# Performance work log

Hardware: AMD Instinct MI355X
Metric: run time of the kernel (lower is better)

## Reference

```python
import jax, jax.numpy as jnp
import numpy as np
from jax import lax

INPUT = 99
HIDDEN = 64
T = 65536


def setup_inputs() -> dict:
    key = jax.random.key(0)
    ks = jax.random.split(key, 8)
    x = jax.random.normal(ks[0], (1, T, INPUT), dtype=jnp.float32)
    # PyTorch LSTM params: weight_ih_l0 [4H, in], weight_hh_l0 [4H, H], biases [4H]
    s = 1.0 / np.sqrt(HIDDEN)
    W_ih = jax.random.uniform(ks[1], (4 * HIDDEN, INPUT), jnp.float32, -s, s)
    W_hh = jax.random.uniform(ks[2], (4 * HIDDEN, HIDDEN), jnp.float32, -s, s)
    b_ih = jax.random.uniform(ks[3], (4 * HIDDEN,), jnp.float32, -s, s)
    b_hh = jax.random.uniform(ks[4], (4 * HIDDEN,), jnp.float32, -s, s)
    # head: Linear(64->32, bias=False), Linear(32->3, bias=True)
    W1 = jax.random.normal(ks[5], (32, HIDDEN), dtype=jnp.float32) * 0.01
    W2 = jax.random.normal(ks[6], (3, 32), dtype=jnp.float32) * 0.01
    b2 = jnp.zeros((3,), dtype=jnp.float32)
    return {"x": x, "W_ih": W_ih, "W_hh": W_hh, "b_ih": b_ih, "b_hh": b_hh,
            "W1": W1, "W2": W2, "b2": b2}


def reference(x, W_ih, W_hh, b_ih, b_hh, W1, W2, b2):
    H = HIDDEN
    # Precompute input projections for all timesteps (one big GEMM).
    # x: [1, T, 99] -> xz: [T, 4H]; x[-1] == last (only) batch row.
    xz = jnp.einsum('td,gd->tg', x[-1], W_ih) + b_ih + b_hh

    def step(carry, z_t):
        h, c = carry
        z = z_t + W_hh @ h  # [4H]
        i, f, g, o = jnp.split(z, 4)  # PyTorch gate order: i, f, g, o
        i = jax.nn.sigmoid(i)
        f = jax.nn.sigmoid(f)
        g = jnp.tanh(g)
        o = jax.nn.sigmoid(o)
        c = f * c + i * g
        h = o * jnp.tanh(c)
        return (h, c), None

    h0 = jnp.zeros((H,), dtype=x.dtype)
    c0 = jnp.zeros((H,), dtype=x.dtype)
    (h_T, _), _ = lax.scan(step, (h0, c0), xz)

    # x[-1, -1] -> last timestep hidden of last batch row, then MLP head
    h = jax.nn.relu(h_T)
    h = jax.nn.relu(W1 @ h)
    out = W2 @ h + b2
    return out[None, :]  # [1, 3]
```

## Files before the change

kernel.cpp:

```cpp
#include <hip/hip_runtime.h>

#define T_STEPS 65536
#define NIN 99
#define HID 64
#define G4 256
#define TS 128
#define PF 8

__device__ __forceinline__ float frcp(float x) { return __builtin_amdgcn_rcpf(x); }
__device__ __forceinline__ float fexp(float x) { return __expf(x); }
__device__ __forceinline__ float sigmoid_f(float x) { return frcp(1.0f + fexp(-x)); }
__device__ __forceinline__ float tanh_f(float x) {
    float ax = fabsf(x);
    float e  = fexp(2.0f * ax);
    float r  = 1.0f - 2.0f * frcp(e + 1.0f);
    return copysignf(r, x);
}
__device__ __forceinline__ float bcast(float v, int lane) {
    return __int_as_float(__builtin_amdgcn_readlane(__float_as_int(v), lane));
}

__global__ __launch_bounds__(256, 1) void xz_kernel(
    const float* __restrict__ x, const float* __restrict__ W_ih,
    const float* __restrict__ b_ih, const float* __restrict__ b_hh,
    float* __restrict__ xz) {
    __shared__ __align__(16) float xs[TS * 100];
    const int g  = threadIdx.x;
    const int t0 = blockIdx.x * TS;

    for (int i = g; i < TS * NIN; i += 256) {
        int tl = i / NIN;
        int j  = i - tl * NIN;
        xs[tl * 100 + j] = x[(size_t)t0 * NIN + i];
    }

    float w[NIN];
#pragma unroll
    for (int j = 0; j < NIN; ++j) w[j] = W_ih[g * NIN + j];
    const float bias = b_ih[g] + b_hh[g];
    __syncthreads();

    for (int tl = 0; tl < TS; ++tl) {
        const float* xr = &xs[tl * 100];
        float a0 = bias, a1 = 0.f, a2 = 0.f, a3 = 0.f;
#pragma unroll
        for (int j4 = 0; j4 < 24; ++j4) {
            float4 xv = *(const float4*)(xr + 4 * j4);
            a0 = fmaf(w[4 * j4 + 0], xv.x, a0);
            a1 = fmaf(w[4 * j4 + 1], xv.y, a1);
            a2 = fmaf(w[4 * j4 + 2], xv.z, a2);
            a3 = fmaf(w[4 * j4 + 3], xv.w, a3);
        }
        a0 = fmaf(w[96], xr[96], a0);
        a1 = fmaf(w[97], xr[97], a1);
        a2 = fmaf(w[98], xr[98], a2);
        xz[(size_t)(t0 + tl) * G4 + g] = (a0 + a1) + (a2 + a3);
    }
}

__global__ __launch_bounds__(256, 1) __attribute__((amdgpu_waves_per_eu(1)))
void lstm_kernel(
    const float* __restrict__ xz, const float* __restrict__ W_hh,
    const float* __restrict__ W1, const float* __restrict__ W2,
    const float* __restrict__ b2, float* __restrict__ out) {
    __shared__ __align__(16) float pbuf[2][4][G4];
    __shared__ float hfin[HID];
    __shared__ float hbuf[32];
    const int tid = threadIdx.x;
    const int l   = tid & 63;
    const int wv  = tid >> 6;
    const int sb  = __builtin_amdgcn_readfirstlane(16 * wv);

    const float* Wb = W_hh + (4 * l) * HID + sb;
    float4 w00 = *(const float4*)(Wb +   0), w01 = *(const float4*)(Wb +   4),
           w02 = *(const float4*)(Wb +   8), w03 = *(const float4*)(Wb +  12);
    float4 w10 = *(const float4*)(Wb +  64), w11 = *(const float4*)(Wb +  68),
           w12 = *(const float4*)(Wb +  72), w13 = *(const float4*)(Wb +  76);
    float4 w20 = *(const float4*)(Wb + 128), w21 = *(const float4*)(Wb + 132),
           w22 = *(const float4*)(Wb + 136), w23 = *(const float4*)(Wb + 140);
    float4 w30 = *(const float4*)(Wb + 192), w31 = *(const float4*)(Wb + 196),
           w32 = *(const float4*)(Wb + 200), w33 = *(const float4*)(Wb + 204);

#define PIN4(v) asm volatile("" : "+v"(v.x), "+v"(v.y), "+v"(v.z), "+v"(v.w))
    PIN4(w00); PIN4(w01); PIN4(w02); PIN4(w03);
    PIN4(w10); PIN4(w11); PIN4(w12); PIN4(w13);
    PIN4(w20); PIN4(w21); PIN4(w22); PIN4(w23);
    PIN4(w30); PIN4(w31); PIN4(w32); PIN4(w33);
#undef PIN4

    float h = 0.0f, c = 0.0f;

    const float* zi = xz + l;
    float4 zcur[PF], znxt[PF];
#pragma unroll
    for (int p = 0; p < PF; ++p) {
        const float* r = zi + (size_t)p * G4;
        zcur[p] = make_float4(r[0], r[64], r[128], r[192]);
        znxt[p] = make_float4(0.f, 0.f, 0.f, 0.f);
    }

#define STEP_J4(J4, W0, W1_, W2_, W3_)                                          \
    {   float hx0 = bcast(h, sb + 4 * J4 + 0);                                  \
        float hx1 = bcast(h, sb + 4 * J4 + 1);                                  \
        float hx2 = bcast(h, sb + 4 * J4 + 2);                                  \
        float hx3 = bcast(h, sb + 4 * J4 + 3);                                  \
        a0 = fmaf(W0.x, hx0, a0); a0 = fmaf(W0.y, hx1, a0);                     \
        a0 = fmaf(W0.z, hx2, a0); a0 = fmaf(W0.w, hx3, a0);                     \
        a1 = fmaf(W1_.x, hx0, a1); a1 = fmaf(W1_.y, hx1, a1);                   \
        a1 = fmaf(W1_.z, hx2, a1); a1 = fmaf(W1_.w, hx3, a1);                   \
        a2 = fmaf(W2_.x, hx0, a2); a2 = fmaf(W2_.y, hx1, a2);                   \
        a2 = fmaf(W2_.z, hx2, a2); a2 = fmaf(W2_.w, hx3, a2);                   \
        a3 = fmaf(W3_.x, hx0, a3); a3 = fmaf(W3_.y, hx1, a3);                   \
        a3 = fmaf(W3_.z, hx2, a3); a3 = fmaf(W3_.w, hx3, a3); }

    for (int tb = 0; tb < T_STEPS; tb += PF) {
        if (tb + PF < T_STEPS) {
#pragma unroll
            for (int p = 0; p < PF; ++p) {
                const float* r = zi + (size_t)(tb + PF + p) * G4;
                znxt[p] = make_float4(r[0], r[64], r[128], r[192]);
            }
        }
#pragma unroll
        for (int u = 0; u < PF; ++u) {
            const int par = u & 1;
            float a0 = 0.f, a1 = 0.f, a2 = 0.f, a3 = 0.f;
            STEP_J4(0, w00, w10, w20, w30)
            STEP_J4(1, w01, w11, w21, w31)
            STEP_J4(2, w02, w12, w22, w32)
            STEP_J4(3, w03, w13, w23, w33)
            *(float4*)(&pbuf[par][wv][4 * l]) = make_float4(a0, a1, a2, a3);
            __syncthreads();

            const float* pb = &pbuf[par][0][0];
            float si = zcur[u].x + ((pb[l]       + pb[G4 + l])       + (pb[2*G4 + l]       + pb[3*G4 + l]));
            float sf = zcur[u].y + ((pb[64 + l]  + pb[G4 + 64 + l])  + (pb[2*G4 + 64 + l]  + pb[3*G4 + 64 + l]));
            float sg = zcur[u].z + ((pb[128 + l] + pb[G4 + 128 + l]) + (pb[2*G4 + 128 + l] + pb[3*G4 + 128 + l]));
            float so = zcur[u].w + ((pb[192 + l] + pb[G4 + 192 + l]) + (pb[2*G4 + 192 + l] + pb[3*G4 + 192 + l]));
            float ig = sigmoid_f(si);
            float fg = sigmoid_f(sf);
            float gg = tanh_f(sg);
            float og = sigmoid_f(so);
            c = fmaf(fg, c, ig * gg);
            h = og * tanh_f(c);
        }
#pragma unroll
        for (int p = 0; p < PF; ++p) zcur[p] = znxt[p];
    }
#undef STEP_J4

    if (tid < HID) hfin[tid] = h;
    __syncthreads();
    if (tid < 32) {
        float s = 0.0f;
#pragma unroll
        for (int j = 0; j < HID; ++j) s += W1[tid * HID + j] * fmaxf(hfin[j], 0.0f);
        hbuf[tid] = fmaxf(s, 0.0f);
    }
    __syncthreads();
    if (tid < 3) {
        float s = b2[tid];
#pragma unroll
        for (int j = 0; j < 32; ++j) s += W2[tid * 32 + j] * hbuf[j];
        out[tid] = s;
    }
}

extern "C" void kernel_launch(void* const* d_in, const int* in_sizes, int n_in,
                              void* d_out, int out_size, void* d_ws, size_t ws_size,
                              hipStream_t stream) {
    const float* x   = (const float*)d_in[0];
    const float* Wih = (const float*)d_in[1];
    const float* Whh = (const float*)d_in[2];
    const float* bih = (const float*)d_in[3];
    const float* bhh = (const float*)d_in[4];
    const float* W1  = (const float*)d_in[5];
    const float* W2  = (const float*)d_in[6];
    const float* b2  = (const float*)d_in[7];
    float* out = (float*)d_out;
    float* xz  = (float*)d_ws;

    xz_kernel<<<T_STEPS / TS, 256, 0, stream>>>(x, Wih, bih, bhh, xz);
    lstm_kernel<<<1, 256, 0, stream>>>(xz, Whh, W1, W2, b2, out);
}
```

Before: 25.93 ms.

## Interleave gate projections per unit and shrink per-step LDS reduction traffic

The xz buffer is rewritten so each hidden unit's four gate values sit contiguously, which lets wave 0 fetch them with a single float4 load, and only wave 0 prefetches them. Each lane now owns unit l across all four gates and adds the input projection into its own accumulator. After the barrier it reads just the three other waves' float4 partials instead of sixteen scalar LDS reads. The plain __syncthreads is replaced by an inline-asm lgkmcnt wait plus s_barrier, which trims the per-step critical path of the serial recurrence but relies on the hand-written asm ordering being correct.

```diff
diff --git a/kernel.cpp b/kernel.cpp
--- a/kernel.cpp
+++ b/kernel.cpp
@@ -20,13 +20,16 @@
     return __int_as_float(__builtin_amdgcn_readlane(__float_as_int(v), lane));
 }
 
+#define BAR_LGKM() asm volatile("s_waitcnt lgkmcnt(0)\n\ts_barrier" ::: "memory")
+
 __global__ __launch_bounds__(256, 1) void xz_kernel(
     const float* __restrict__ x, const float* __restrict__ W_ih,
     const float* __restrict__ b_ih, const float* __restrict__ b_hh,
-    float* __restrict__ xz) {
+    float* __restrict__ xz2) {
     __shared__ __align__(16) float xs[TS * 100];
     const int g  = threadIdx.x;
     const int t0 = blockIdx.x * TS;
+    const int unit = g & 63, d = g >> 6;
 
     for (int i = g; i < TS * NIN; i += 256) {
         int tl = i / NIN;
@@ -54,16 +57,16 @@
         a0 = fmaf(w[96], xr[96], a0);
         a1 = fmaf(w[97], xr[97], a1);
         a2 = fmaf(w[98], xr[98], a2);
-        xz[(size_t)(t0 + tl) * G4 + g] = (a0 + a1) + (a2 + a3);
+        xz2[(size_t)(t0 + tl) * G4 + unit * 4 + d] = (a0 + a1) + (a2 + a3);
     }
 }
 
 __global__ __launch_bounds__(256, 1) __attribute__((amdgpu_waves_per_eu(1)))
 void lstm_kernel(
-    const float* __restrict__ xz, const float* __restrict__ W_hh,
+    const float* __restrict__ xz2, const float* __restrict__ W_hh,
     const float* __restrict__ W1, const float* __restrict__ W2,
     const float* __restrict__ b2, float* __restrict__ out) {
-    __shared__ __align__(16) float pbuf[2][4][G4];
+    __shared__ __align__(16) float4 pbuf[2][4][HID];
     __shared__ float hfin[HID];
     __shared__ float hbuf[32];
     const int tid = threadIdx.x;
@@ -71,72 +74,72 @@
     const int wv  = tid >> 6;
     const int sb  = __builtin_amdgcn_readfirstlane(16 * wv);
 
-    const float* Wb = W_hh + (4 * l) * HID + sb;
-    float4 w00 = *(const float4*)(Wb +   0), w01 = *(const float4*)(Wb +   4),
-           w02 = *(const float4*)(Wb +   8), w03 = *(const float4*)(Wb +  12);
-    float4 w10 = *(const float4*)(Wb +  64), w11 = *(const float4*)(Wb +  68),
-           w12 = *(const float4*)(Wb +  72), w13 = *(const float4*)(Wb +  76);
-    float4 w20 = *(const float4*)(Wb + 128), w21 = *(const float4*)(Wb + 132),
-           w22 = *(const float4*)(Wb + 136), w23 = *(const float4*)(Wb + 140);
-    float4 w30 = *(const float4*)(Wb + 192), w31 = *(const float4*)(Wb + 196),
-           w32 = *(const float4*)(Wb + 200), w33 = *(const float4*)(Wb + 204);
+    const float* Wb = W_hh + l * HID + sb;
+    float4 wi0 = *(const float4*)(Wb +     0), wi1 = *(const float4*)(Wb +     4),
+           wi2 = *(const float4*)(Wb +     8), wi3 = *(const float4*)(Wb +    12);
+    float4 wf0 = *(const float4*)(Wb +  4096), wf1 = *(const float4*)(Wb +  4100),
+           wf2 = *(const float4*)(Wb +  4104), wf3 = *(const float4*)(Wb +  4108);
+    float4 wg0 = *(const float4*)(Wb +  8192), wg1 = *(const float4*)(Wb +  8196),
+           wg2 = *(const float4*)(Wb +  8200), wg3 = *(const float4*)(Wb +  8204);
+    float4 wo0 = *(const float4*)(Wb + 12288), wo1 = *(const float4*)(Wb + 12292),
+           wo2 = *(const float4*)(Wb + 12296), wo3 = *(const float4*)(Wb + 12300);
 
 #define PIN4(v) asm volatile("" : "+v"(v.x), "+v"(v.y), "+v"(v.z), "+v"(v.w))
-    PIN4(w00); PIN4(w01); PIN4(w02); PIN4(w03);
-    PIN4(w10); PIN4(w11); PIN4(w12); PIN4(w13);
-    PIN4(w20); PIN4(w21); PIN4(w22); PIN4(w23);
-    PIN4(w30); PIN4(w31); PIN4(w32); PIN4(w33);
+    PIN4(wi0); PIN4(wi1); PIN4(wi2); PIN4(wi3);
+    PIN4(wf0); PIN4(wf1); PIN4(wf2); PIN4(wf3);
+    PIN4(wg0); PIN4(wg1); PIN4(wg2); PIN4(wg3);
+    PIN4(wo0); PIN4(wo1); PIN4(wo2); PIN4(wo3);
 #undef PIN4
 
     float h = 0.0f, c = 0.0f;
 
-    const float* zi = xz + l;
+    const float* zi = xz2 + 4 * l;
     float4 zcur[PF], znxt[PF];
+    if (wv == 0) {
 #pragma unroll
-    for (int p = 0; p < PF; ++p) {
-        const float* r = zi + (size_t)p * G4;
-        zcur[p] = make_float4(r[0], r[64], r[128], r[192]);
-        znxt[p] = make_float4(0.f, 0.f, 0.f, 0.f);
+        for (int p = 0; p < PF; ++p) zcur[p] = *(const float4*)(zi + (size_t)p * G4);
     }
 
-#define STEP_J4(J4, W0, W1_, W2_, W3_)                                          \
+#define STEP_J4(J4, WI, WF, WG, WO)                                             \
     {   float hx0 = bcast(h, sb + 4 * J4 + 0);                                  \
         float hx1 = bcast(h, sb + 4 * J4 + 1);                                  \
         float hx2 = bcast(h, sb + 4 * J4 + 2);                                  \
         float hx3 = bcast(h, sb + 4 * J4 + 3);                                  \
-        a0 = fmaf(W0.x, hx0, a0); a0 = fmaf(W0.y, hx1, a0);                     \
-        a0 = fmaf(W0.z, hx2, a0); a0 = fmaf(W0.w, hx3, a0);                     \
-        a1 = fmaf(W1_.x, hx0, a1); a1 = fmaf(W1_.y, hx1, a1);                   \
-        a1 = fmaf(W1_.z, hx2, a1); a1 = fmaf(W1_.w, hx3, a1);                   \
-        a2 = fmaf(W2_.x, hx0, a2); a2 = fmaf(W2_.y, hx1, a2);                   \
-        a2 = fmaf(W2_.z, hx2, a2); a2 = fmaf(W2_.w, hx3, a2);                   \
-        a3 = fmaf(W3_.x, hx0, a3); a3 = fmaf(W3_.y, hx1, a3);                   \
-        a3 = fmaf(W3_.z, hx2, a3); a3 = fmaf(W3_.w, hx3, a3); }
+        ai = fmaf(WI.x, hx0, ai); ai = fmaf(WI.y, hx1, ai);                     \
+        ai = fmaf(WI.z, hx2, ai); ai = fmaf(WI.w, hx3, ai);                     \
+        af = fmaf(WF.x, hx0, af); af = fmaf(WF.y, hx1, af);                     \
+        af = fmaf(WF.z, hx2, af); af = fmaf(WF.w, hx3, af);                     \
+        ag = fmaf(WG.x, hx0, ag); ag = fmaf(WG.y, hx1, ag);                     \
+        ag = fmaf(WG.z, hx2, ag); ag = fmaf(WG.w, hx3, ag);                     \
+        ao = fmaf(WO.x, hx0, ao); ao = fmaf(WO.y, hx1, ao);                     \
+        ao = fmaf(WO.z, hx2, ao); ao = fmaf(WO.w, hx3, ao); }
 
     for (int tb = 0; tb < T_STEPS; tb += PF) {
-        if (tb + PF < T_STEPS) {
+        if (wv == 0 && tb + PF < T_STEPS) {
 #pragma unroll
-            for (int p = 0; p < PF; ++p) {
-                const float* r = zi + (size_t)(tb + PF + p) * G4;
-                znxt[p] = make_float4(r[0], r[64], r[128], r[192]);
-            }
+            for (int p = 0; p < PF; ++p)
+                znxt[p] = *(const float4*)(zi + (size_t)(tb + PF + p) * G4);
         }
 #pragma unroll
         for (int u = 0; u < PF; ++u) {
             const int par = u & 1;
-            float a0 = 0.f, a1 = 0.f, a2 = 0.f, a3 = 0.f;
-            STEP_J4(0, w00, w10, w20, w30)
-            STEP_J4(1, w01, w11, w21, w31)
-            STEP_J4(2, w02, w12, w22, w32)
-            STEP_J4(3, w03, w13, w23, w33)
-            *(float4*)(&pbuf[par][wv][4 * l]) = make_float4(a0, a1, a2, a3);
-            __syncthreads();
+            float ai, af, ag, ao;
+            if (wv == 0) { ai = zcur[u].x; af = zcur[u].y; ag = zcur[u].z; ao = zcur[u].w; }
+            else         { ai = 0.f; af = 0.f; ag = 0.f; ao = 0.f; }
+            STEP_J4(0, wi0, wf0, wg0, wo0)
+            STEP_J4(1, wi1, wf1, wg1, wo1)
+            STEP_J4(2, wi2, wf2, wg2, wo2)
+            STEP_J4(3, wi3, wf3, wg3, wo3)
+            pbuf[par][wv][l] = make_float4(ai, af, ag, ao);
+            BAR_LGKM();
 
-            const float* pb = &pbuf[par][0][0];
-            float si = zcur[u].x + ((pb[l]       + pb[G4 + l])       + (pb[2*G4 + l]       + pb[3*G4 + l]));
-            float sf = zcur[u].y + ((pb[64 + l]  + pb[G4 + 64 + l])  + (pb[2*G4 + 64 + l]  + pb[3*G4 + 64 + l]));
-            float sg = zcur[u].z + ((pb[128 + l] + pb[G4 + 128 + l]) + (pb[2*G4 + 128 + l] + pb[3*G4 + 128 + l]));
-            float so = zcur[u].w + ((pb[192 + l] + pb[G4 + 192 + l]) + (pb[2*G4 + 192 + l] + pb[3*G4 + 192 + l]));
+            float4 r0 = pbuf[par][(wv + 1) & 3][l];
+            float4 r1 = pbuf[par][(wv + 2) & 3][l];
+            float4 r2 = pbuf[par][(wv + 3) & 3][l];
+            float si = (ai + r0.x) + (r1.x + r2.x);
+            float sf = (af + r0.y) + (r1.y + r2.y);
+            float sg = (ag + r0.z) + (r1.z + r2.z);
+            float so = (ao + r0.w) + (r1.w + r2.w);
             float ig = sigmoid_f(si);
             float fg = sigmoid_f(sf);
             float gg = tanh_f(sg);
@@ -144,8 +147,10 @@
             c = fmaf(fg, c, ig * gg);
             h = og * tanh_f(c);
         }
+        if (wv == 0) {
 #pragma unroll
-        for (int p = 0; p < PF; ++p) zcur[p] = znxt[p];
+            for (int p = 0; p < PF; ++p) zcur[p] = znxt[p];
+        }
     }
 #undef STEP_J4
 
@@ -178,8 +183,8 @@
     const float* W2  = (const float*)d_in[6];
     const float* b2  = (const float*)d_in[7];
     float* out = (float*)d_out;
-    float* xz  = (float*)d_ws;
+    float* xz2 = (float*)d_ws;
 
-    xz_kernel<<<T_STEPS / TS, 256, 0, stream>>>(x, Wih, bih, bhh, xz);
-    lstm_kernel<<<1, 256, 0, stream>>>(xz, Whh, W1, W2, b2, out);
+    xz_kernel<<<T_STEPS / TS, 256, 0, stream>>>(x, Wih, bih, bhh, xz2);
+    lstm_kernel<<<1, 256, 0, stream>>>(xz2, Whh, W1, W2, b2, out);
 }
```

After: 22.91 ms. 11.7% less time.
